# Performance work log

Hardware: AMD Instinct MI355X
Metric: run time of the kernel (lower is better)

The kernel has to match this reference:

```python
import jax, jax.numpy as jnp
import numpy as np

N_NODES = 100000
IN_CH = 128
HID = 128   # 2 * out_channels
OUT = 64
N_EDGES = 1600000


def gcn_conv(x, W, b, src, dst, n_nodes):
    """PyG GCNConv: add self-loops, symmetric normalization D^-1/2 (A+I) D^-1/2 X W + b."""
    h = x @ W  # [N, F_out]
    ones = jnp.ones(dst.shape[0], dtype=h.dtype)
    # degree of target nodes, +1 for self loop
    deg = jax.ops.segment_sum(ones, dst, num_segments=n_nodes) + 1.0
    dinv = jnp.where(deg > 0, jax.lax.rsqrt(deg), 0.0)  # [N]
    norm = dinv[src] * dinv[dst]  # [E]
    agg = jax.ops.segment_sum(h[src] * norm[:, None], dst, num_segments=n_nodes)
    # self-loop contribution: norm_ii = dinv_i^2 (avoids materializing extra edges)
    agg = agg + h * (dinv * dinv)[:, None]
    return agg + b


def setup_inputs() -> dict:
    key = jax.random.key(0)
    ks = jax.random.split(key, 8)
    x = jax.random.normal(ks[0], (N_NODES, IN_CH), dtype=jnp.float32)
    edge_index = jax.random.randint(ks[1], (2, N_EDGES), 0, N_NODES, dtype=jnp.int64)
    # Glorot-style params
    W1 = jax.random.normal(ks[2], (IN_CH, HID), dtype=jnp.float32) / np.sqrt(IN_CH)
    b1 = jnp.zeros((HID,), dtype=jnp.float32)
    W_mu = jax.random.normal(ks[3], (HID, OUT), dtype=jnp.float32) / np.sqrt(HID)
    b_mu = jnp.zeros((OUT,), dtype=jnp.float32)
    W_ls = jax.random.normal(ks[4], (HID, OUT), dtype=jnp.float32) / np.sqrt(HID)
    b_ls = jnp.zeros((OUT,), dtype=jnp.float32)
    return {"x": x, "edge_index": edge_index, "W1": W1, "b1": b1,
            "W_mu": W_mu, "b_mu": b_mu, "W_ls": W_ls, "b_ls": b_ls}


def reference(x, edge_index, W1, b1, W_mu, b_mu, W_ls, b_ls):
    src, dst = edge_index[0], edge_index[1]
    n = x.shape[0]
    h = jax.nn.relu(gcn_conv(x, W1, b1, src, dst, n))
    mu = gcn_conv(h, W_mu, b_mu, src, dst, n)
    logstd = gcn_conv(h, W_ls, b_ls, src, dst, n)
    return (mu, logstd)
```

## Files before the change

### kernel.cpp

```cpp
#include <hip/hip_runtime.h>
#include <hip/hip_bf16.h>
#include <stdint.h>

#define N_NODES 100000
#define IN_CH   128
#define HID     128
#define OUT_CH  64
#define N_EDGES 1600000

#define NB    196
#define NBLK  250
#define EPB   6400


__device__ __forceinline__ unsigned short f2bf(float f) {
    unsigned int u = __float_as_uint(f);
    u = (u + 0x7fffu + ((u >> 16) & 1u)) >> 16;
    return (unsigned short)u;
}
__device__ __forceinline__ float bfl(unsigned int u) { return __uint_as_float(u << 16); }
__device__ __forceinline__ float bfh(unsigned int u) { return __uint_as_float(u & 0xffff0000u); }


__global__ __launch_bounds__(256) void k_phaseA(const int* __restrict__ dst,
                                                int* __restrict__ Cm) {
    __shared__ int hist[NB];
    int blk = blockIdx.x, t = threadIdx.x;
    if (t < NB) hist[t] = 0;
    __syncthreads();
    int base = blk * EPB;
#pragma unroll 5
    for (int k = 0; k < EPB / 256; k++) {
        int d = dst[base + k * 256 + t];
        atomicAdd(&hist[d >> 9], 1);
    }
    __syncthreads();
    if (t < NB) Cm[blk * NB + t] = hist[t];
}

__global__ __launch_bounds__(256) void k_scanCm(int* __restrict__ Cm,
                                                int* __restrict__ bktBase) {
    __shared__ int sdata[256];
    int t = threadIdx.x;
    int run = 0;
    if (t < NB) {
        for (int blk = 0; blk < NBLK; blk++) {
            int idx = blk * NB + t;
            int v = Cm[idx];
            Cm[idx] = run;
            run += v;
        }
    }
    int s = (t < NB) ? run : 0;
    sdata[t] = s;
    __syncthreads();
    int val = s;
    for (int off = 1; off < 256; off <<= 1) {
        int tmp = (t >= off) ? sdata[t - off] : 0;
        __syncthreads();
        val += tmp;
        sdata[t] = val;
        __syncthreads();
    }
    if (t < NB) bktBase[t] = val - s;
    if (t == 0) bktBase[NB] = N_EDGES;
}

__global__ __launch_bounds__(256) void k_phaseB(const int* __restrict__ src,
                                                const int* __restrict__ dst,
                                                const int* __restrict__ Cm,
                                                const int* __restrict__ bktBase,
                                                unsigned int* __restrict__ bucketed) {
    __shared__ int offs[NB];
    int blk = blockIdx.x, t = threadIdx.x;
    if (t < NB) offs[t] = Cm[blk * NB + t] + bktBase[t];
    __syncthreads();
    int base = blk * EPB;
#pragma unroll 5
    for (int k = 0; k < EPB / 256; k++) {
        int e = base + k * 256 + t;
        int d = dst[e];
        int sv = src[e];
        int pos = atomicAdd(&offs[d >> 9], 1);
        bucketed[pos] = ((unsigned int)sv << 9) | (unsigned int)(d & 511);
    }
}

__global__ __launch_bounds__(512) void k_phaseC(const unsigned int* __restrict__ bucketed,
                                                const int* __restrict__ bktBase,
                                                int* __restrict__ rowptr,
                                                float* __restrict__ dinvg,
                                                int* __restrict__ csr_src) {
    __shared__ int cnt[512];
    __shared__ int cur[512];
    __shared__ int sdata[512];
    int b = blockIdx.x, t = threadIdx.x;
    int base = bktBase[b], endR = bktBase[b + 1];
    int nodeBase = b << 9;
    int nNodes = N_NODES - nodeBase;
    if (nNodes > 512) nNodes = 512;

    cnt[t] = 0;
    __syncthreads();
    for (int e = base + t; e < endR; e += 512)
        atomicAdd(&cnt[bucketed[e] & 511], 1);
    __syncthreads();

    int s = cnt[t];
    sdata[t] = s;
    __syncthreads();
    int val = s;
    for (int off = 1; off < 512; off <<= 1) {
        int tmp = (t >= off) ? sdata[t - off] : 0;
        __syncthreads();
        val += tmp;
        sdata[t] = val;
        __syncthreads();
    }
    cur[t] = val - s;
    if (t < nNodes) {
        rowptr[nodeBase + t] = base + val - s;
        dinvg[nodeBase + t] = rsqrtf((float)s + 1.0f);
    }
    if (b == NB - 1 && t == 0) rowptr[N_NODES] = N_EDGES;
    __syncthreads();

    for (int e = base + t; e < endR; e += 512) {
        unsigned int u = bucketed[e];
        int pos = base + atomicAdd(&cur[u & 511], 1);
        csr_src[pos] = (int)(u >> 9);
    }
}


__global__ __launch_bounds__(256) void k_pack(const float* __restrict__ Wmu,
                                              const float* __restrict__ Wls,
                                              float* __restrict__ Wcat) {
    int idx = blockIdx.x * 256 + threadIdx.x;
    if (idx < 128 * 128) {
        int k = idx >> 7, c = idx & 127;
        Wcat[idx] = (c < 64) ? Wmu[k * 64 + c] : Wls[k * 64 + (c - 64)];
    }
}

#define GROWS 32
__global__ __launch_bounds__(256) void k_gemm(const float* __restrict__ X,
                                              const float* __restrict__ W,
                                              unsigned short* __restrict__ Y) {
    __shared__ float sW[128 * 128];
    __shared__ float sX[GROWS * 128];
    int t = threadIdx.x;
    {
        const float4* W4 = (const float4*)W;
        float4* sW4 = (float4*)sW;
#pragma unroll
        for (int j = 0; j < 16; j++) sW4[t + 256 * j] = W4[t + 256 * j];
        const float4* X4 = (const float4*)(X + (size_t)blockIdx.x * GROWS * 128);
        float4* sX4 = (float4*)sX;
#pragma unroll
        for (int j = 0; j < 4; j++) sX4[t + 256 * j] = X4[t + 256 * j];
    }
    __syncthreads();

    int tx = t & 31;
    int ty = t >> 5;
    float acc[4][4] = {};

#pragma unroll 2
    for (int k0 = 0; k0 < 128; k0 += 4) {
        float4 xq[4];
#pragma unroll
        for (int r = 0; r < 4; r++)
            xq[r] = *(const float4*)&sX[(ty * 4 + r) * 128 + k0];
#pragma unroll
        for (int kk = 0; kk < 4; kk++) {
            float4 w = *(const float4*)&sW[(k0 + kk) * 128 + tx * 4];
#pragma unroll
            for (int r = 0; r < 4; r++) {
                float xv = ((const float*)&xq[r])[kk];
                acc[r][0] = fmaf(xv, w.x, acc[r][0]);
                acc[r][1] = fmaf(xv, w.y, acc[r][1]);
                acc[r][2] = fmaf(xv, w.z, acc[r][2]);
                acc[r][3] = fmaf(xv, w.w, acc[r][3]);
            }
        }
    }
    unsigned short* Yb = Y + (size_t)blockIdx.x * GROWS * 128;
#pragma unroll
    for (int r = 0; r < 4; r++) {
        ushort4 o;
        o.x = f2bf(acc[r][0]);
        o.y = f2bf(acc[r][1]);
        o.z = f2bf(acc[r][2]);
        o.w = f2bf(acc[r][3]);
        *(ushort4*)&Yb[(ty * 4 + r) * 128 + tx * 4] = o;
    }
}


__global__ __launch_bounds__(256) void k_agg1(const unsigned short* __restrict__ h0,
                                              const int* __restrict__ rowptr,
                                              const int* __restrict__ csr_src,
                                              const float* __restrict__ dinv,
                                              const float* __restrict__ b1,
                                              float* __restrict__ h) {
    int lane = threadIdx.x & 63;
    int i = __builtin_amdgcn_readfirstlane(blockIdx.x * 4 + (threadIdx.x >> 6));
    int c2 = lane * 2;
    float di = dinv[i];
    unsigned int sv = *(const unsigned int*)(h0 + (size_t)i * 128 + c2);
    float ax = bfl(sv) * di * di, ay = bfh(sv) * di * di;
    int beg = rowptr[i], end = rowptr[i + 1];
    for (int p = beg; p < end; p += 8) {
        int s[8]; float n[8]; unsigned int r[8];
#pragma unroll
        for (int j = 0; j < 8; j++) {
            int q = p + j;
            s[j] = csr_src[q < end ? q : end - 1];
        }
#pragma unroll
        for (int j = 0; j < 8; j++) n[j] = dinv[s[j]];
#pragma unroll
        for (int j = 0; j < 8; j++)
            r[j] = *(const unsigned int*)(h0 + (size_t)s[j] * 128 + c2);
#pragma unroll
        for (int j = 0; j < 8; j++) n[j] = (p + j < end) ? n[j] * di : 0.f;
#pragma unroll
        for (int j = 0; j < 8; j++) {
            ax = fmaf(bfl(r[j]), n[j], ax);
            ay = fmaf(bfh(r[j]), n[j], ay);
        }
    }
    ax += b1[c2];
    ay += b1[c2 + 1];
    ax = ax > 0.f ? ax : 0.f;
    ay = ay > 0.f ? ay : 0.f;
    *(float2*)(h + (size_t)i * 128 + c2) = make_float2(ax, ay);
}

__global__ __launch_bounds__(256) void k_agg2(const unsigned short* __restrict__ tt,
                                              const int* __restrict__ rowptr,
                                              const int* __restrict__ csr_src,
                                              const float* __restrict__ dinv,
                                              const float* __restrict__ bmu,
                                              const float* __restrict__ bls,
                                              float* __restrict__ out) {
    int lane = threadIdx.x & 63;
    int i = __builtin_amdgcn_readfirstlane(blockIdx.x * 4 + (threadIdx.x >> 6));
    int c2 = lane * 2;
    float di = dinv[i];
    unsigned int sv = *(const unsigned int*)(tt + (size_t)i * 128 + c2);
    float ax = bfl(sv) * di * di, ay = bfh(sv) * di * di;
    int beg = rowptr[i], end = rowptr[i + 1];
    for (int p = beg; p < end; p += 8) {
        int s[8]; float n[8]; unsigned int r[8];
#pragma unroll
        for (int j = 0; j < 8; j++) {
            int q = p + j;
            s[j] = csr_src[q < end ? q : end - 1];
        }
#pragma unroll
        for (int j = 0; j < 8; j++) n[j] = dinv[s[j]];
#pragma unroll
        for (int j = 0; j < 8; j++)
            r[j] = *(const unsigned int*)(tt + (size_t)s[j] * 128 + c2);
#pragma unroll
        for (int j = 0; j < 8; j++) n[j] = (p + j < end) ? n[j] * di : 0.f;
#pragma unroll
        for (int j = 0; j < 8; j++) {
            ax = fmaf(bfl(r[j]), n[j], ax);
            ay = fmaf(bfh(r[j]), n[j], ay);
        }
    }
    if (lane < 32) {
        int c = c2;
        *(float2*)(out + (size_t)i * 64 + c) =
            make_float2(ax + bmu[c], ay + bmu[c + 1]);
    } else {
        int c = c2 - 64;
        *(float2*)(out + (size_t)N_NODES * 64 + (size_t)i * 64 + c) =
            make_float2(ax + bls[c], ay + bls[c + 1]);
    }
}


extern "C" void kernel_launch(void* const* d_in, const int* in_sizes, int n_in,
                              void* d_out, int out_size, void* d_ws, size_t ws_size,
                              hipStream_t stream) {
    const float* x    = (const float*)d_in[0];
    const int*   ei   = (const int*)d_in[1];
    const float* W1   = (const float*)d_in[2];
    const float* b1   = (const float*)d_in[3];
    const float* Wmu  = (const float*)d_in[4];
    const float* bmu  = (const float*)d_in[5];
    const float* Wls  = (const float*)d_in[6];
    const float* bls  = (const float*)d_in[7];
    const int* src = ei;
    const int* dst = ei + N_EDGES;

    char* p = (char*)d_ws;
    unsigned short* bufA = (unsigned short*)p; p += (size_t)N_NODES * 128 * 2;
    float* bufB    = (float*)p; p += (size_t)N_NODES * 128 * 4;
    float* Wcat    = (float*)p; p += 128 * 128 * 4;
    int*   Cm      = (int*)p;   p += (size_t)NBLK * NB * 4;
    int*   bktBase = (int*)p;   p += 256 * 4;
    int*   rowptr  = (int*)p;   p += 400016;
    float* dinv    = (float*)p; p += 400000;
    unsigned int* bucketed = (unsigned int*)p; p += (size_t)N_EDGES * 4;
    int*   csr_src = (int*)p;   p += (size_t)N_EDGES * 4;

    k_phaseA<<<NBLK, 256, 0, stream>>>(dst, Cm);
    k_scanCm<<<1, 256, 0, stream>>>(Cm, bktBase);
    k_phaseB<<<NBLK, 256, 0, stream>>>(src, dst, Cm, bktBase, bucketed);
    k_phaseC<<<NB, 512, 0, stream>>>(bucketed, bktBase, rowptr, dinv, csr_src);

    k_pack<<<64, 256, 0, stream>>>(Wmu, Wls, Wcat);

    k_gemm<<<N_NODES / GROWS, 256, 0, stream>>>(x, W1, bufA);
    k_agg1<<<N_NODES / 4, 256, 0, stream>>>(bufA, rowptr, csr_src, dinv, b1, bufB);

    k_gemm<<<N_NODES / GROWS, 256, 0, stream>>>(bufB, Wcat, bufA);
    k_agg2<<<N_NODES / 4, 256, 0, stream>>>(bufA, rowptr, csr_src, dinv,
                                            bmu, bls, (float*)d_out);
}
```

Before: 399.3 us.

## Use bf16 MFMA for both dense GEMMs and store hidden layer as bf16

Replaces the fp32 FMA shared-memory GEMM with a bf16 MFMA (16x16x32) GEMM over 128-row tiles, with weights pre-transposed and converted to bf16 in one prep kernel. The first-layer aggregation now writes its ReLU output as packed bf16 instead of fp32, halving that intermediate's write and the second GEMM's read. Input x is converted to bf16 while it is staged into padded shared memory. This targets the ALU cost of the dense transforms and memory traffic, at the price of bf16 rounding on inputs, weights and hidden activations, and uncoalesced 2-byte scattered output stores.

```diff
diff --git a/kernel.cpp b/kernel.cpp
--- a/kernel.cpp
+++ b/kernel.cpp
@@ -11,6 +11,9 @@
 #define NB    196
 #define NBLK  250
 #define EPB   6400
+
+typedef __attribute__((ext_vector_type(8))) short  bf16x8;
+typedef __attribute__((ext_vector_type(4))) float  f32x4;
 
 
 __device__ __forceinline__ unsigned short f2bf(float f) {
@@ -133,68 +136,104 @@
 }
 
 
-__global__ __launch_bounds__(256) void k_pack(const float* __restrict__ Wmu,
-                                              const float* __restrict__ Wls,
-                                              float* __restrict__ Wcat) {
+__global__ __launch_bounds__(256) void k_prepW(const float* __restrict__ W1,
+                                               const float* __restrict__ Wmu,
+                                               const float* __restrict__ Wls,
+                                               unsigned short* __restrict__ Wt1,
+                                               unsigned short* __restrict__ WtC) {
     int idx = blockIdx.x * 256 + threadIdx.x;
-    if (idx < 128 * 128) {
-        int k = idx >> 7, c = idx & 127;
-        Wcat[idx] = (c < 64) ? Wmu[k * 64 + c] : Wls[k * 64 + (c - 64)];
-    }
-}
-
-#define GROWS 32
-__global__ __launch_bounds__(256) void k_gemm(const float* __restrict__ X,
-                                              const float* __restrict__ W,
-                                              unsigned short* __restrict__ Y) {
-    __shared__ float sW[128 * 128];
-    __shared__ float sX[GROWS * 128];
+    int n = idx >> 7, k = idx & 127;
+    Wt1[idx] = f2bf(W1[k * 128 + n]);
+    WtC[idx] = f2bf((n < 64) ? Wmu[k * 64 + n] : Wls[k * 64 + (n - 64)]);
+}
+
+
+#define LDA 136
+
+__device__ __forceinline__ void gemm_compute(const unsigned short* sA,
+                                             const unsigned short* __restrict__ Wt,
+                                             unsigned short* __restrict__ Y,
+                                             int R0, int t) {
+    int wv = t >> 6, l = t & 63;
+    int quad = l >> 4, lm = l & 15;
+
+    bf16x8 a[2][4];
+#pragma unroll
+    for (int mt = 0; mt < 2; mt++)
+#pragma unroll
+        for (int ks = 0; ks < 4; ks++)
+            a[mt][ks] = *(const bf16x8*)(sA + (wv * 32 + mt * 16 + lm) * LDA +
+                                         ks * 32 + quad * 8);
+
+    f32x4 acc[2][8] = {};
+#pragma unroll
+    for (int nt = 0; nt < 8; nt++) {
+        bf16x8 b[4];
+        const unsigned short* Wp = Wt + (nt * 16 + lm) * 128 + quad * 8;
+#pragma unroll
+        for (int ks = 0; ks < 4; ks++)
+            b[ks] = *(const bf16x8*)(Wp + ks * 32);
+#pragma unroll
+        for (int mt = 0; mt < 2; mt++) {
+            f32x4 c = acc[mt][nt];
+#pragma unroll
+            for (int ks = 0; ks < 4; ks++)
+                c = __builtin_amdgcn_mfma_f32_16x16x32_bf16(a[mt][ks], b[ks], c, 0, 0, 0);
+            acc[mt][nt] = c;
+        }
+    }
+
+    int rbase = R0 + wv * 32 + quad * 4;
+#pragma unroll
+    for (int mt = 0; mt < 2; mt++)
+#pragma unroll
+        for (int nt = 0; nt < 8; nt++)
+#pragma unroll
+            for (int reg = 0; reg < 4; reg++) {
+                int row = rbase + mt * 16 + reg;
+                if (row < N_NODES)
+                    Y[(size_t)row * 128 + nt * 16 + lm] = f2bf(acc[mt][nt][reg]);
+            }
+}
+
+__global__ __launch_bounds__(256) void k_gemm1(const float* __restrict__ X,
+                                               const unsigned short* __restrict__ Wt,
+                                               unsigned short* __restrict__ Y) {
+    __shared__ unsigned short sA[128 * LDA];
     int t = threadIdx.x;
-    {
-        const float4* W4 = (const float4*)W;
-        float4* sW4 = (float4*)sW;
-#pragma unroll
-        for (int j = 0; j < 16; j++) sW4[t + 256 * j] = W4[t + 256 * j];
-        const float4* X4 = (const float4*)(X + (size_t)blockIdx.x * GROWS * 128);
-        float4* sX4 = (float4*)sX;
-#pragma unroll
-        for (int j = 0; j < 4; j++) sX4[t + 256 * j] = X4[t + 256 * j];
-    }
-    __syncthreads();
-
-    int tx = t & 31;
-    int ty = t >> 5;
-    float acc[4][4] = {};
-
-#pragma unroll 2
-    for (int k0 = 0; k0 < 128; k0 += 4) {
-        float4 xq[4];
-#pragma unroll
-        for (int r = 0; r < 4; r++)
-            xq[r] = *(const float4*)&sX[(ty * 4 + r) * 128 + k0];
-#pragma unroll
-        for (int kk = 0; kk < 4; kk++) {
-            float4 w = *(const float4*)&sW[(k0 + kk) * 128 + tx * 4];
-#pragma unroll
-            for (int r = 0; r < 4; r++) {
-                float xv = ((const float*)&xq[r])[kk];
-                acc[r][0] = fmaf(xv, w.x, acc[r][0]);
-                acc[r][1] = fmaf(xv, w.y, acc[r][1]);
-                acc[r][2] = fmaf(xv, w.z, acc[r][2]);
-                acc[r][3] = fmaf(xv, w.w, acc[r][3]);
-            }
-        }
-    }
-    unsigned short* Yb = Y + (size_t)blockIdx.x * GROWS * 128;
-#pragma unroll
-    for (int r = 0; r < 4; r++) {
+    int R0 = blockIdx.x * 128;
+    int row = t >> 1, colb = (t & 1) * 64;
+    bool valid = (R0 + row) < N_NODES;
+    const float* Xr = X + (size_t)(R0 + row) * 128 + colb;
+    unsigned short* dp = sA + row * LDA + colb;
+#pragma unroll
+    for (int j = 0; j < 16; j++) {
+        float4 v = valid ? *(const float4*)(Xr + j * 4) : make_float4(0.f, 0.f, 0.f, 0.f);
         ushort4 o;
-        o.x = f2bf(acc[r][0]);
-        o.y = f2bf(acc[r][1]);
-        o.z = f2bf(acc[r][2]);
-        o.w = f2bf(acc[r][3]);
-        *(ushort4*)&Yb[(ty * 4 + r) * 128 + tx * 4] = o;
-    }
+        o.x = f2bf(v.x); o.y = f2bf(v.y); o.z = f2bf(v.z); o.w = f2bf(v.w);
+        *(ushort4*)(dp + j * 4) = o;
+    }
+    __syncthreads();
+    gemm_compute(sA, Wt, Y, R0, t);
+}
+
+__global__ __launch_bounds__(256) void k_gemm2(const unsigned short* __restrict__ Xb,
+                                               const unsigned short* __restrict__ Wt,
+                                               unsigned short* __restrict__ Y) {
+    __shared__ unsigned short sA[128 * LDA];
+    int t = threadIdx.x;
+    int R0 = blockIdx.x * 128;
+    int row = t >> 1, colb = (t & 1) * 64;
+    bool valid = (R0 + row) < N_NODES;
+    const unsigned short* Xr = Xb + (size_t)(R0 + row) * 128 + colb;
+    unsigned short* dp = sA + row * LDA + colb;
+#pragma unroll
+    for (int j = 0; j < 8; j++) {
+        uint4 v = valid ? *(const uint4*)(Xr + j * 8) : make_uint4(0u, 0u, 0u, 0u);
+        *(uint4*)(dp + j * 8) = v;
+    }
+    __syncthreads();
+    gemm_compute(sA, Wt, Y, R0, t);
 }
 
 
@@ -203,7 +242,7 @@
                                               const int* __restrict__ csr_src,
                                               const float* __restrict__ dinv,
                                               const float* __restrict__ b1,
-                                              float* __restrict__ h) {
+                                              unsigned short* __restrict__ hb) {
     int lane = threadIdx.x & 63;
     int i = __builtin_amdgcn_readfirstlane(blockIdx.x * 4 + (threadIdx.x >> 6));
     int c2 = lane * 2;
@@ -235,7 +274,8 @@
     ay += b1[c2 + 1];
     ax = ax > 0.f ? ax : 0.f;
     ay = ay > 0.f ? ay : 0.f;
-    *(float2*)(h + (size_t)i * 128 + c2) = make_float2(ax, ay);
+    unsigned int pk = ((unsigned int)f2bf(ay) << 16) | (unsigned int)f2bf(ax);
+    *(unsigned int*)(hb + (size_t)i * 128 + c2) = pk;
 }
 
 __global__ __launch_bounds__(256) void k_agg2(const unsigned short* __restrict__ tt,
@@ -300,8 +340,9 @@
 
     char* p = (char*)d_ws;
     unsigned short* bufA = (unsigned short*)p; p += (size_t)N_NODES * 128 * 2;
-    float* bufB    = (float*)p; p += (size_t)N_NODES * 128 * 4;
-    float* Wcat    = (float*)p; p += 128 * 128 * 4;
+    unsigned short* bufH = (unsigned short*)p; p += (size_t)N_NODES * 128 * 2;
+    unsigned short* Wt1  = (unsigned short*)p; p += 128 * 128 * 2;
+    unsigned short* WtC  = (unsigned short*)p; p += 128 * 128 * 2;
     int*   Cm      = (int*)p;   p += (size_t)NBLK * NB * 4;
     int*   bktBase = (int*)p;   p += 256 * 4;
     int*   rowptr  = (int*)p;   p += 400016;
@@ -314,12 +355,14 @@
     k_phaseB<<<NBLK, 256, 0, stream>>>(src, dst, Cm, bktBase, bucketed);
     k_phaseC<<<NB, 512, 0, stream>>>(bucketed, bktBase, rowptr, dinv, csr_src);
 
-    k_pack<<<64, 256, 0, stream>>>(Wmu, Wls, Wcat);
-
-    k_gemm<<<N_NODES / GROWS, 256, 0, stream>>>(x, W1, bufA);
-    k_agg1<<<N_NODES / 4, 256, 0, stream>>>(bufA, rowptr, csr_src, dinv, b1, bufB);
-
-    k_gemm<<<N_NODES / GROWS, 256, 0, stream>>>(bufB, Wcat, bufA);
+    k_prepW<<<64, 256, 0, stream>>>(W1, Wmu, Wls, Wt1, WtC);
+
+    int gblk = (N_NODES + 127) / 128;
+
+    k_gemm1<<<gblk, 256, 0, stream>>>(x, Wt1, bufA);
+    k_agg1<<<N_NODES / 4, 256, 0, stream>>>(bufA, rowptr, csr_src, dinv, b1, bufH);
+
+    k_gemm2<<<gblk, 256, 0, stream>>>(bufH, WtC, bufA);
     k_agg2<<<N_NODES / 4, 256, 0, stream>>>(bufA, rowptr, csr_src, dinv,
                                             bmu, bls, (float*)d_out);
 }
```

Measured after the change: 353.2 us. 11.5% less time.
